# Optimization experiments

Hardware: AMD Instinct MI355X
Metric: run time of the kernel (lower is better)

The kernel has to match this reference:

```python
import jax, jax.numpy as jnp
import numpy as np

T, D, E, DE = 50000, 128, 1600000, 3
EPS = 1e-5


def setup_inputs() -> dict:
    key = jax.random.key(0)
    ks = jax.random.split(key, 8)
    H = jax.random.normal(ks[0], (T, D), dtype=jnp.float32)
    edge_index = jax.random.randint(ks[1], (2, E), 0, T, dtype=jnp.int64)
    edge_attr = jax.random.normal(ks[2], (E, DE), dtype=jnp.float32)
    # phi: Linear(D+DE -> D), GELU, Linear(D -> D)
    s1 = 1.0 / np.sqrt(D + DE)
    s2 = 1.0 / np.sqrt(D)
    W1 = jax.random.uniform(ks[3], (D + DE, D), minval=-s1, maxval=s1, dtype=jnp.float32)
    b1 = jax.random.uniform(ks[4], (D,), minval=-s1, maxval=s1, dtype=jnp.float32)
    W2 = jax.random.uniform(ks[5], (D, D), minval=-s2, maxval=s2, dtype=jnp.float32)
    b2 = jax.random.uniform(ks[6], (D,), minval=-s2, maxval=s2, dtype=jnp.float32)
    gamma = jnp.ones((D,), dtype=jnp.float32)
    beta = jnp.zeros((D,), dtype=jnp.float32)
    return {"H": H, "edge_index": edge_index, "edge_attr": edge_attr,
            "W1": W1, "b1": b1, "W2": W2, "b2": b2, "gamma": gamma, "beta": beta}


def reference(H, edge_index, edge_attr, W1, b1, W2, b2, gamma, beta):
    src, dst = edge_index[0], edge_index[1]
    Hj = H[src]                                   # [E, D] gather
    feat = jnp.concatenate([Hj, edge_attr], axis=-1)  # [E, D+DE]
    h = jax.nn.gelu(feat @ W1 + b1, approximate=False)
    m = h @ W2 + b2                               # [E, D] messages
    agg = jax.ops.segment_sum(m, dst, num_segments=H.shape[0])  # scatter-add
    x = H + agg
    mu = jnp.mean(x, axis=-1, keepdims=True)
    var = jnp.mean((x - mu) ** 2, axis=-1, keepdims=True)
    return (x - mu) * jax.lax.rsqrt(var + EPS) * gamma + beta
```

## Files before the change

### kernel.cpp

```cpp
#include <hip/hip_runtime.h>
#include <hip/hip_bf16.h>

typedef unsigned short u16;
typedef unsigned int u32;
typedef __attribute__((ext_vector_type(8))) __bf16 bf16x8;
typedef __attribute__((ext_vector_type(4))) float f32x4;

#define NT 50000
#define NEDGE 1600000
#define GRID2 2048
#define NPAIR 4096
#define NBIN 50176

__device__ __forceinline__ u16 f2bf(float f) {
  unsigned x = __float_as_uint(f);
  x += 0x7fffu + ((x >> 16) & 1u);
  return (u16)(x >> 16);
}

__device__ __forceinline__ int swz(int row, int col) {
  return (row << 7) + (col ^ ((row & 7) << 3));
}

__device__ __forceinline__ float gelu(float v) {
  float u = v * v;
  float arg = v * __builtin_fmaf(-0.1029434f, u, -2.3022082f);
  float e = __builtin_amdgcn_exp2f(arg);
  return v * __builtin_amdgcn_rcpf(1.0f + e);
}

__device__ __forceinline__ void atomAddF32(float* p, float v) {
#if defined(__has_builtin)
#if __has_builtin(__builtin_amdgcn_global_atomic_fadd_f32)
  __builtin_amdgcn_global_atomic_fadd_f32((__attribute__((address_space(1))) float*)p, v);
  return;
#endif
#endif
  atomicAdd(p, v);
}


__global__ void prep_all(const float* __restrict__ H, u16* __restrict__ Hb,
                         const float* __restrict__ W1, const float* __restrict__ W2,
                         u16* __restrict__ wsw, const float* __restrict__ b1,
                         u16* __restrict__ wx, u32* __restrict__ cnt) {
  int bid = blockIdx.x, tid = threadIdx.x;
  if (bid < 3125) {
    int t = bid * 256 + tid;
    const float4* s = (const float4*)H + (long)t * 2;
    float4 a = s[0], c = s[1];
    int4 pk;
    pk.x = f2bf(a.x) | ((int)f2bf(a.y) << 16);
    pk.y = f2bf(a.z) | ((int)f2bf(a.w) << 16);
    pk.z = f2bf(c.x) | ((int)f2bf(c.y) << 16);
    pk.w = f2bf(c.z) | ((int)f2bf(c.w) << 16);
    ((int4*)Hb)[t] = pk;
  } else if (bid < 3253) {
    int t = (bid - 3125) * 256 + tid;
    int m = t >> 14;
    int p = t & 16383;
    int row = p >> 7;
    int colq = p & 127;
    int k = colq ^ ((row & 7) << 3);
    const float* W = m ? W2 : W1;
    wsw[t] = f2bf(W[k * 128 + row]);
  } else if (bid < 3257) {
    int t = (bid - 3253) * 256 + tid;
    int row = t >> 3, j = t & 7;
    float v = 0.f;
    if (j < 3) v = W1[(128 + j) * 128 + row];
    else if (j == 3) v = b1[row];
    wx[t] = f2bf(v);
  } else if (bid < 3453) {
    int t = (bid - 3257) * 256 + tid;
    if (t < NBIN) cnt[t] = 0;
  } else {
    if (tid < 16) ((int4*)(Hb + (long)NT * 128))[tid] = make_int4(0, 0, 0, 0);
  }
}

__global__ void copy_h(const float4* __restrict__ H, float4* __restrict__ out) {
  int t = blockIdx.x * 256 + threadIdx.x;
  out[t] = H[t];
}


__global__ void hist_g(const int* __restrict__ ei, u32* __restrict__ cnt) {
  int e = blockIdx.x * 256 + threadIdx.x;
  atomicAdd(&cnt[ei[NEDGE + e]], 1u);
}

__global__ void scan_blk(u32* __restrict__ cnt, u32* __restrict__ btot) {
  __shared__ u32 ls[1024];
  int tid = threadIdx.x;
  int bin = blockIdx.x * 1024 + tid;
  u32 c = cnt[bin];
  ls[tid] = c;
  __syncthreads();
  for (int o = 1; o < 1024; o <<= 1) {
    u32 t = (tid >= o) ? ls[tid - o] : 0u;
    __syncthreads();
    ls[tid] += t;
    __syncthreads();
  }
  cnt[bin] = ls[tid] - c;
  if (tid == 1023) btot[blockIdx.x] = ls[1023];
}

__global__ void scan_btot(u32* __restrict__ btot) {
  if (threadIdx.x == 0) {
    u32 run = 0;
    for (int i = 0; i < 49; ++i) { u32 t = btot[i]; btot[i] = run; run += t; }
  }
}

__global__ void fin_base(const u32* __restrict__ cnt, const u32* __restrict__ btot,
                         u32* __restrict__ base, u32* __restrict__ pos) {
  int bin = blockIdx.x * 256 + threadIdx.x;
  if (bin < NT) {
    u32 v = cnt[bin] + btot[bin >> 10];
    base[bin] = v;
    pos[bin] = v;
  }
  if (bin == NT) base[NT] = NEDGE;
}

__global__ void scatter_g(const int* __restrict__ ei, const float* __restrict__ ea,
                          u32* __restrict__ pos, uint2* __restrict__ rec) {
  int e = blockIdx.x * 256 + threadIdx.x;
  int d = ei[NEDGE + e];
  int s = ei[e];
  float e0 = ea[e * 3 + 0], e1 = ea[e * 3 + 1], e2 = ea[e * 3 + 2];
  u32 p = atomicAdd(&pos[d], 1u);
  rec[p] = make_uint2((u32)s | ((u32)f2bf(e0) << 16),
                      (u32)f2bf(e1) | ((u32)f2bf(e2) << 16));
}


__launch_bounds__(256)
__global__ void msg_agg(const u16* __restrict__ Hb,
                        const u16* __restrict__ wsw,
                        const u16* __restrict__ wx,
                        const u32* __restrict__ base,
                        const uint2* __restrict__ rec,
                        u16* __restrict__ hsb) {
  __shared__ __align__(16) u16 lw1x[128 * 8];

  const int tid = threadIdx.x;
  if (tid < 128) ((int4*)lw1x)[tid] = ((const int4*)wx)[tid];
  __syncthreads();

  const int wv = tid >> 6, lane = tid & 63;
  const int l15 = lane & 15, l4 = lane >> 4;

  const int gid = blockIdx.x * 4 + wv;
  const int pair = gid >> 1;
  const int nh = gid & 1;

  bf16x8 af[4][4];
#pragma unroll
  for (int nt = 0; nt < 4; ++nt)
#pragma unroll
    for (int ks = 0; ks < 4; ++ks)
      af[nt][ks] = *(const bf16x8*)&wsw[swz((nh * 4 + nt) * 16 + l15, ks * 32 + l4 * 8)];

  const int d0 = (int)(((long)pair * NT) / NPAIR);
  const int d1i = (int)(((long)(pair + 1) * NT) / NPAIR);
  const int nd = d1i - d0;

  for (int b = 0; b < nd; ++b) {
    const int start = (int)base[d0 + b];
    const int cnt = (int)base[d0 + b + 1] - start;

    float racc[4][4];
#pragma unroll
    for (int nt = 0; nt < 4; ++nt)
#pragma unroll
      for (int r = 0; r < 4; ++r) racc[nt][r] = 0.f;

    const int ntile = (cnt + 15) >> 4;
    uint2 r2c = make_uint2(0, 0);
    if (ntile > 0) {
      int i0 = (l15 < cnt) ? l15 : cnt - 1;
      r2c = rec[start + i0];
    }

    for (int t = 0; t < ntile; ++t) {
      int inx = (t + 1) * 16 + l15;
      if (inx >= cnt) inx = cnt - 1;
      uint2 r2n = rec[start + inx];

      const bool valid = (t * 16 + l15) < cnt;
      int src = valid ? (int)(r2c.x & 0xFFFFu) : NT;
      u32 x0 = 0u, x1 = 0u;
      if (l4 == 0 && valid) {
        x0 = (r2c.x >> 16) | (r2c.y << 16);
        x1 = (r2c.y >> 16) | 0x3F800000u;
      }
      int4 xbi = make_int4((int)x0, (int)x1, 0, 0);
      bf16x8 bfrx = *(bf16x8*)&xbi;

      bf16x8 bfc[4];
      {
        const u16* hr = Hb + (long)src * 128;
#pragma unroll
        for (int ks = 0; ks < 4; ++ks)
          bfc[ks] = *(const bf16x8*)(hr + ks * 32 + l4 * 8);
      }

#pragma unroll
      for (int nt = 0; nt < 4; ++nt) {
        bf16x8 afrx = *(const bf16x8*)&lw1x[((nh * 4 + nt) * 16 + l15) * 8];
        f32x4 acc = (f32x4){0.f, 0.f, 0.f, 0.f};
#pragma unroll
        for (int ks = 0; ks < 4; ++ks)
          acc = __builtin_amdgcn_mfma_f32_16x16x32_bf16(bfc[ks], af[nt][ks], acc, 0, 0, 0);
        acc = __builtin_amdgcn_mfma_f32_16x16x32_bf16(bfrx, afrx, acc, 0, 0, 0);
#pragma unroll
        for (int r = 0; r < 4; ++r)
          racc[nt][r] += gelu(acc[r]);
      }
      r2c = r2n;
    }

    float sv[4];
#pragma unroll
    for (int nt = 0; nt < 4; ++nt) {
      float s = racc[nt][0] + racc[nt][1] + racc[nt][2] + racc[nt][3];
      s += __shfl_xor(s, 16);
      s += __shfl_xor(s, 32);
      sv[nt] = s;
    }
    float sa = (l4 == 0) ? sv[0] : (l4 == 1) ? sv[1] : (l4 == 2) ? sv[2] : sv[3];
    u16* hrow = hsb + (long)(d0 + b) * 128;
    hrow[nh * 64 + l4 * 16 + l15] = f2bf(sa);
  }
}


__launch_bounds__(256)
__global__ void gemm_ln(const u16* __restrict__ hsb,
                        const float* __restrict__ H,
                        const float* __restrict__ b2,
                        const u16* __restrict__ wsw,
                        const u32* __restrict__ base,
                        const float* __restrict__ gamma,
                        const float* __restrict__ beta,
                        float* __restrict__ out) {
  __shared__ __align__(16) u16 lw2[16384];
  const int tid = threadIdx.x;
  {
    const int4* g = (const int4*)wsw + 2048;
    int4* d2 = (int4*)lw2;
#pragma unroll
    for (int i = 0; i < 8; ++i) { int c = tid + i * 256; d2[c] = g[c]; }
  }
  __syncthreads();

  const int wv = tid >> 6, lane = tid & 63;
  const int l15 = lane & 15, l4 = lane >> 4;
  const int r0 = (blockIdx.x * 4 + wv) * 16;

  bf16x8 ha[4];
#pragma unroll
  for (int ks = 0; ks < 4; ++ks)
    ha[ks] = *(const bf16x8*)(hsb + (long)(r0 + l15) * 128 + ks * 32 + l4 * 8);

  float cntr[4];
#pragma unroll
  for (int r = 0; r < 4; ++r) {
    int row = r0 + l4 * 4 + r;
    if (row > NT - 1) row = NT - 1;
    cntr[r] = (float)(base[row + 1] - base[row]);
  }

  float xv[8][4];
#pragma unroll
  for (int nt = 0; nt < 8; ++nt) {
    bf16x8 bfr2[4];
#pragma unroll
    for (int ks = 0; ks < 4; ++ks)
      bfr2[ks] = *(const bf16x8*)&lw2[swz(nt * 16 + l15, ks * 32 + l4 * 8)];
    float b2v = b2[nt * 16 + l15];
    f32x4 acc = (f32x4){0.f, 0.f, 0.f, 0.f};
#pragma unroll
    for (int ks = 0; ks < 4; ++ks)
      acc = __builtin_amdgcn_mfma_f32_16x16x32_bf16(ha[ks], bfr2[ks], acc, 0, 0, 0);
#pragma unroll
    for (int r = 0; r < 4; ++r) {
      int row = r0 + l4 * 4 + r;
      long o = (long)((row < NT) ? row : NT - 1) * 128 + nt * 16 + l15;
      xv[nt][r] = H[o] + acc[r] + cntr[r] * b2v;
    }
  }

  float mu[4], rs[4];
#pragma unroll
  for (int r = 0; r < 4; ++r) {
    float s = 0.f;
#pragma unroll
    for (int nt = 0; nt < 8; ++nt) s += xv[nt][r];
    s += __shfl_xor(s, 1); s += __shfl_xor(s, 2);
    s += __shfl_xor(s, 4); s += __shfl_xor(s, 8);
    mu[r] = s * (1.0f / 128.0f);
    float q = 0.f;
#pragma unroll
    for (int nt = 0; nt < 8; ++nt) {
      float d = xv[nt][r] - mu[r];
      q += d * d;
    }
    q += __shfl_xor(q, 1); q += __shfl_xor(q, 2);
    q += __shfl_xor(q, 4); q += __shfl_xor(q, 8);
    rs[r] = rsqrtf(q * (1.0f / 128.0f) + 1e-5f);
  }

#pragma unroll
  for (int nt = 0; nt < 8; ++nt) {
    int col = nt * 16 + l15;
    float g = gamma[col], bb = beta[col];
#pragma unroll
    for (int r = 0; r < 4; ++r) {
      int row = r0 + l4 * 4 + r;
      if (row < NT)
        out[(long)row * 128 + col] = (xv[nt][r] - mu[r]) * rs[r] * g + bb;
    }
  }
}


template <int BF16H>
__launch_bounds__(256, 1)
__global__ void msg_atomic(const float* __restrict__ H,
                           const u16* __restrict__ Hb,
                           const int* __restrict__ ei,
                           const float* __restrict__ ea,
                           const float* __restrict__ W1,
                           const float* __restrict__ b1,
                           const float* __restrict__ b2,
                           const u16* __restrict__ wsw,
                           float* __restrict__ out) {
  __shared__ __align__(16) u16 lw1[16384];
  __shared__ __align__(16) u16 lw2[16384];
  __shared__ __align__(16) u16 lh[4 * 2048];
  __shared__ __align__(16) float lep[5][128];

  const int tid = threadIdx.x;
  {
    const int4* g = (const int4*)wsw;
    int4* d1 = (int4*)lw1;
    int4* d2 = (int4*)lw2;
#pragma unroll
    for (int i = 0; i < 8; ++i) {
      int c = tid + i * 256;
      d1[c] = g[c];
      d2[c] = g[2048 + c];
    }
  }
  if (tid < 128) {
    lep[0][tid] = b1[tid];
    lep[1][tid] = W1[128 * 128 + tid];
    lep[2][tid] = W1[129 * 128 + tid];
    lep[3][tid] = W1[130 * 128 + tid];
    lep[4][tid] = b2[tid];
  }
  __syncthreads();

  const int wv = tid >> 6, lane = tid & 63;
  const int l15 = lane & 15, l4 = lane >> 4;
  u16* lhw = lh + wv * 2048;
  const int gwid = blockIdx.x * 4 + wv;

  for (int g = gwid; g < NEDGE / 16; g += 4096) {
    const int eb = g * 16;
    int src = ei[eb + l15];
    float ea0 = ea[(eb + l15) * 3 + 0], ea1 = ea[(eb + l15) * 3 + 1], ea2 = ea[(eb + l15) * 3 + 2];

    bf16x8 bfr[4];
    if (BF16H) {
      const u16* hr = Hb + (long)src * 128;
#pragma unroll
      for (int ks = 0; ks < 4; ++ks)
        bfr[ks] = *(const bf16x8*)(hr + ks * 32 + l4 * 8);
    } else {
      const float* hr = H + (long)src * 128;
#pragma unroll
      for (int ks = 0; ks < 4; ++ks) {
        float4 a = *(const float4*)(hr + ks * 32 + l4 * 8);
        float4 c = *(const float4*)(hr + ks * 32 + l4 * 8 + 4);
        int4 pk;
        pk.x = f2bf(a.x) | ((int)f2bf(a.y) << 16);
        pk.y = f2bf(a.z) | ((int)f2bf(a.w) << 16);
        pk.z = f2bf(c.x) | ((int)f2bf(c.y) << 16);
        pk.w = f2bf(c.z) | ((int)f2bf(c.w) << 16);
        bfr[ks] = *(bf16x8*)&pk;
      }
    }

#pragma unroll
    for (int nt = 0; nt < 8; ++nt) {
      bf16x8 afr[4];
#pragma unroll
      for (int ks = 0; ks < 4; ++ks)
        afr[ks] = *(const bf16x8*)&lw1[swz(nt * 16 + l15, ks * 32 + l4 * 8)];
      f32x4 acc = (f32x4){0.f, 0.f, 0.f, 0.f};
#pragma unroll
      for (int ks = 0; ks < 4; ++ks)
        acc = __builtin_amdgcn_mfma_f32_16x16x32_bf16(afr[ks], bfr[ks], acc, 0, 0, 0);
      f32x4 b1v = *(const f32x4*)&lep[0][nt * 16 + l4 * 4];
      f32x4 w0v = *(const f32x4*)&lep[1][nt * 16 + l4 * 4];
      f32x4 w1v = *(const f32x4*)&lep[2][nt * 16 + l4 * 4];
      f32x4 w2v = *(const f32x4*)&lep[3][nt * 16 + l4 * 4];
      float hv[4];
#pragma unroll
      for (int r = 0; r < 4; ++r) {
        float v = acc[r] + b1v[r] + ea0 * w0v[r] + ea1 * w1v[r] + ea2 * w2v[r];
        hv[r] = gelu(v);
      }
      int2 hp;
      hp.x = f2bf(hv[0]) | ((int)f2bf(hv[1]) << 16);
      hp.y = f2bf(hv[2]) | ((int)f2bf(hv[3]) << 16);
      *(int2*)&lhw[swz(l15, nt * 16 + l4 * 4)] = hp;
    }

    asm volatile("" ::: "memory");

    bf16x8 ha[4];
#pragma unroll
    for (int ks = 0; ks < 4; ++ks)
      ha[ks] = *(const bf16x8*)&lhw[swz(l15, ks * 32 + l4 * 8)];
    int drow[4];
#pragma unroll
    for (int r = 0; r < 4; ++r) drow[r] = ei[NEDGE + eb + l4 * 4 + r];

#pragma unroll
    for (int nt = 0; nt < 8; ++nt) {
      bf16x8 bfr2[4];
#pragma unroll
      for (int ks = 0; ks < 4; ++ks)
        bfr2[ks] = *(const bf16x8*)&lw2[swz(nt * 16 + l15, ks * 32 + l4 * 8)];
      float b2v = lep[4][nt * 16 + l15];
      f32x4 acc = (f32x4){0.f, 0.f, 0.f, 0.f};
#pragma unroll
      for (int ks = 0; ks < 4; ++ks)
        acc = __builtin_amdgcn_mfma_f32_16x16x32_bf16(ha[ks], bfr2[ks], acc, 0, 0, 0);
#pragma unroll
      for (int r = 0; r < 4; ++r)
        atomAddF32(out + (long)drow[r] * 128 + nt * 16 + l15, acc[r] + b2v);
    }
  }
}

__global__ void ln_rows(float* __restrict__ out, const float* __restrict__ gamma,
                        const float* __restrict__ beta) {
  int wave = threadIdx.x >> 6, lane = threadIdx.x & 63;
  int row = blockIdx.x * 4 + wave;
  float2 v = *(const float2*)(out + (long)row * 128 + lane * 2);
  float s = v.x + v.y;
#pragma unroll
  for (int off = 32; off; off >>= 1) s += __shfl_xor(s, off);
  float mu = s * (1.0f / 128.0f);
  float dx = v.x - mu, dy = v.y - mu;
  float q = dx * dx + dy * dy;
#pragma unroll
  for (int off = 32; off; off >>= 1) q += __shfl_xor(q, off);
  float rs = rsqrtf(q * (1.0f / 128.0f) + 1e-5f);
  float2 g = *(const float2*)(gamma + lane * 2);
  float2 b = *(const float2*)(beta + lane * 2);
  float2 o;
  o.x = dx * rs * g.x + b.x;
  o.y = dy * rs * g.y + b.y;
  *(float2*)(out + (long)row * 128 + lane * 2) = o;
}

extern "C" void kernel_launch(void* const* d_in, const int* in_sizes, int n_in,
                              void* d_out, int out_size, void* d_ws, size_t ws_size,
                              hipStream_t stream) {
  const float* H   = (const float*)d_in[0];
  const int* ei    = (const int*)d_in[1];
  const float* ea  = (const float*)d_in[2];
  const float* W1  = (const float*)d_in[3];
  const float* b1  = (const float*)d_in[4];
  const float* W2  = (const float*)d_in[5];
  const float* b2  = (const float*)d_in[6];
  const float* gam = (const float*)d_in[7];
  const float* bet = (const float*)d_in[8];
  float* out = (float*)d_out;

  char* ws = (char*)d_ws;
  u16* wsw   = (u16*)ws;
  u16* wx    = (u16*)(ws + 65536);
  u16* Hb    = (u16*)(ws + 67584);
  u32* cnt   = (u32*)(ws + 12867840);
  u32* base  = (u32*)(ws + 13068544);
  u32* pos   = (u32*)(ws + 13268560);
  u32* btot  = (u32*)(ws + 13468560);
  uint2* rec = (uint2*)(ws + 13468832);
  u16* hsb   = (u16*)(ws + 26268832);
  const size_t NEED_FULL = 39081120;
  const size_t NEED_HB = 12867840;

  if (ws_size >= NEED_FULL) {
    prep_all<<<3454, 256, 0, stream>>>(H, Hb, W1, W2, wsw, b1, wx, cnt);
    hist_g<<<6250, 256, 0, stream>>>(ei, cnt);
    scan_blk<<<49, 1024, 0, stream>>>(cnt, btot);
    scan_btot<<<1, 64, 0, stream>>>(btot);
    fin_base<<<196, 256, 0, stream>>>(cnt, btot, base, pos);
    scatter_g<<<6250, 256, 0, stream>>>(ei, ea, pos, rec);
    msg_agg<<<GRID2, 256, 0, stream>>>(Hb, wsw, wx, base, rec, hsb);
    gemm_ln<<<782, 256, 0, stream>>>(hsb, H, b2, wsw, base, gam, bet, out);
  } else if (ws_size >= NEED_HB) {
    prep_all<<<3454, 256, 0, stream>>>(H, Hb, W1, W2, wsw, b1, wx, cnt);
    copy_h<<<6250, 256, 0, stream>>>((const float4*)H, (float4*)out);
    msg_atomic<1><<<1024, 256, 0, stream>>>(H, Hb, ei, ea, W1, b1, b2, wsw, out);
    ln_rows<<<12500, 256, 0, stream>>>(out, gam, bet);
  } else {
    copy_h<<<6250, 256, 0, stream>>>((const float4*)H, (float4*)out);
    msg_atomic<0><<<1024, 256, 0, stream>>>(H, Hb, ei, ea, W1, b1, b2, wsw, out);
    ln_rows<<<12500, 256, 0, stream>>>(out, gam, bet);
  }
}
```

Before: 372.8 us.

## Edge-balanced msg_agg with packed multi-destination tiles and fused btot scan

Rewrites msg_agg so each wave takes an equal slice of the CSR edge range, found by binary search over base, instead of a fixed range of destinations. Tiles of 16 edges can now span several destinations, and per-row masks split the GELU outputs among them. This removes the padding waste from partial tiles and the load imbalance between waves. Each wave now covers all 128 output columns and reads W1 fragments from global or cache per tile rather than holding them in registers. It also prefetches the next tile's H rows and folds the single-thread btot scan into fin_base, saving one launch. The costs are more register pressure, repeated weight loads, and extra masking FMAs per tile.

```diff
diff --git a/kernel.cpp b/kernel.cpp
--- a/kernel.cpp
+++ b/kernel.cpp
@@ -9,7 +9,7 @@
 #define NT 50000
 #define NEDGE 1600000
 #define GRID2 2048
-#define NPAIR 4096
+#define TOTW 8192
 #define NBIN 50176
 
 __device__ __forceinline__ u16 f2bf(float f) {
@@ -107,18 +107,18 @@
   if (tid == 1023) btot[blockIdx.x] = ls[1023];
 }
 
-__global__ void scan_btot(u32* __restrict__ btot) {
-  if (threadIdx.x == 0) {
-    u32 run = 0;
-    for (int i = 0; i < 49; ++i) { u32 t = btot[i]; btot[i] = run; run += t; }
-  }
-}
-
 __global__ void fin_base(const u32* __restrict__ cnt, const u32* __restrict__ btot,
                          u32* __restrict__ base, u32* __restrict__ pos) {
-  int bin = blockIdx.x * 256 + threadIdx.x;
+  __shared__ u32 bpre[49];
+  int tid = threadIdx.x;
+  if (tid == 0) {
+    u32 run = 0;
+    for (int i = 0; i < 49; ++i) { u32 t = btot[i]; bpre[i] = run; run += t; }
+  }
+  __syncthreads();
+  int bin = blockIdx.x * 256 + tid;
   if (bin < NT) {
-    u32 v = cnt[bin] + btot[bin >> 10];
+    u32 v = cnt[bin] + bpre[bin >> 10];
     base[bin] = v;
     pos[bin] = v;
   }
@@ -137,7 +137,7 @@
 }
 
 
-__launch_bounds__(256)
+__launch_bounds__(256, 1)
 __global__ void msg_agg(const u16* __restrict__ Hb,
                         const u16* __restrict__ wsw,
                         const u16* __restrict__ wx,
@@ -152,88 +152,127 @@
 
   const int wv = tid >> 6, lane = tid & 63;
   const int l15 = lane & 15, l4 = lane >> 4;
-
   const int gid = blockIdx.x * 4 + wv;
-  const int pair = gid >> 1;
-  const int nh = gid & 1;
-
-  bf16x8 af[4][4];
-#pragma unroll
-  for (int nt = 0; nt < 4; ++nt)
+
+  const long t0 = ((long)gid * NEDGE) / TOTW;
+  const long t1 = ((long)(gid + 1) * NEDGE) / TOTW;
+  int lo = 0, hi = NT;
+  while (lo < hi) { int mid = (lo + hi) >> 1; if ((long)base[mid] < t0) lo = mid + 1; else hi = mid; }
+  const int d0 = lo;
+  hi = NT;
+  while (lo < hi) { int mid = (lo + hi) >> 1; if ((long)base[mid] < t1) lo = mid + 1; else hi = mid; }
+  const int d1i = lo;
+  if (d0 >= d1i) return;
+
+  const int pstart = (int)base[d0];
+  const int pend = (int)base[d1i];
+  int bcur = d0;
+  int tlo = pstart;
+  int cend = (int)base[d0 + 1];
+
+  float racc[8][4];
+#pragma unroll
+  for (int nt = 0; nt < 8; ++nt)
+#pragma unroll
+    for (int r = 0; r < 4; ++r) racc[nt][r] = 0.f;
+
+  int pp = pstart + l15;
+  bool vc0 = pp < pend;
+  if (!vc0) pp = pend - 1;
+  uint2 r2c = rec[pp];
+  bf16x8 bfc[4];
+  {
+    int src0 = vc0 ? (int)(r2c.x & 0xFFFFu) : NT;
+    const u16* hr = Hb + (long)src0 * 128;
 #pragma unroll
     for (int ks = 0; ks < 4; ++ks)
-      af[nt][ks] = *(const bf16x8*)&wsw[swz((nh * 4 + nt) * 16 + l15, ks * 32 + l4 * 8)];
-
-  const int d0 = (int)(((long)pair * NT) / NPAIR);
-  const int d1i = (int)(((long)(pair + 1) * NT) / NPAIR);
-  const int nd = d1i - d0;
-
-  for (int b = 0; b < nd; ++b) {
-    const int start = (int)base[d0 + b];
-    const int cnt = (int)base[d0 + b + 1] - start;
-
-    float racc[4][4];
-#pragma unroll
-    for (int nt = 0; nt < 4; ++nt)
-#pragma unroll
-      for (int r = 0; r < 4; ++r) racc[nt][r] = 0.f;
-
-    const int ntile = (cnt + 15) >> 4;
-    uint2 r2c = make_uint2(0, 0);
-    if (ntile > 0) {
-      int i0 = (l15 < cnt) ? l15 : cnt - 1;
-      r2c = rec[start + i0];
-    }
-
-    for (int t = 0; t < ntile; ++t) {
-      int inx = (t + 1) * 16 + l15;
-      if (inx >= cnt) inx = cnt - 1;
-      uint2 r2n = rec[start + inx];
-
-      const bool valid = (t * 16 + l15) < cnt;
-      int src = valid ? (int)(r2c.x & 0xFFFFu) : NT;
-      u32 x0 = 0u, x1 = 0u;
-      if (l4 == 0 && valid) {
-        x0 = (r2c.x >> 16) | (r2c.y << 16);
-        x1 = (r2c.y >> 16) | 0x3F800000u;
+      bfc[ks] = *(const bf16x8*)(hr + ks * 32 + l4 * 8);
+  }
+
+  for (int p0 = pstart; p0 < pend; p0 += 16) {
+    int pn = p0 + 16 + l15;
+    bool vn = pn < pend;
+    if (!vn) pn = pend - 1;
+    uint2 r2n = rec[pn];
+    bf16x8 bfn[4];
+    {
+      int srcn = vn ? (int)(r2n.x & 0xFFFFu) : NT;
+      const u16* hr = Hb + (long)srcn * 128;
+#pragma unroll
+      for (int ks = 0; ks < 4; ++ks)
+        bfn[ks] = *(const bf16x8*)(hr + ks * 32 + l4 * 8);
+    }
+
+    bool vc = (p0 + l15) < pend;
+    u32 x0 = 0u, x1 = 0u;
+    if (l4 == 0 && vc) {
+      x0 = (r2c.x >> 16) | (r2c.y << 16);
+      x1 = (r2c.y >> 16) | 0x3F800000u;
+    }
+    int4 xbi = make_int4((int)x0, (int)x1, 0, 0);
+    bf16x8 bfrx = *(bf16x8*)&xbi;
+
+    float gv[8][4];
+#pragma unroll
+    for (int nt = 0; nt < 8; ++nt) {
+      bf16x8 afrx = *(const bf16x8*)&lw1x[(nt * 16 + l15) * 8];
+      f32x4 acc = (f32x4){0.f, 0.f, 0.f, 0.f};
+#pragma unroll
+      for (int ks = 0; ks < 4; ++ks) {
+        bf16x8 afr = *(const bf16x8*)&wsw[swz(nt * 16 + l15, ks * 32 + l4 * 8)];
+        acc = __builtin_amdgcn_mfma_f32_16x16x32_bf16(bfc[ks], afr, acc, 0, 0, 0);
       }
-      int4 xbi = make_int4((int)x0, (int)x1, 0, 0);
-      bf16x8 bfrx = *(bf16x8*)&xbi;
-
-      bf16x8 bfc[4];
-      {
-        const u16* hr = Hb + (long)src * 128;
-#pragma unroll
-        for (int ks = 0; ks < 4; ++ks)
-          bfc[ks] = *(const bf16x8*)(hr + ks * 32 + l4 * 8);
+      acc = __builtin_amdgcn_mfma_f32_16x16x32_bf16(bfrx, afrx, acc, 0, 0, 0);
+#pragma unroll
+      for (int r = 0; r < 4; ++r)
+        gv[nt][r] = gelu(acc[r]);
+    }
+
+    int thi = p0 + 16;
+    if (thi > pend) thi = pend;
+    while (true) {
+      float m[4];
+#pragma unroll
+      for (int r = 0; r < 4; ++r) {
+        int pos = p0 + l4 * 4 + r;
+        m[r] = (pos >= tlo && pos < cend) ? 1.0f : 0.0f;
       }
-
-#pragma unroll
-      for (int nt = 0; nt < 4; ++nt) {
-        bf16x8 afrx = *(const bf16x8*)&lw1x[((nh * 4 + nt) * 16 + l15) * 8];
-        f32x4 acc = (f32x4){0.f, 0.f, 0.f, 0.f};
-#pragma unroll
-        for (int ks = 0; ks < 4; ++ks)
-          acc = __builtin_amdgcn_mfma_f32_16x16x32_bf16(bfc[ks], af[nt][ks], acc, 0, 0, 0);
-        acc = __builtin_amdgcn_mfma_f32_16x16x32_bf16(bfrx, afrx, acc, 0, 0, 0);
+#pragma unroll
+      for (int nt = 0; nt < 8; ++nt)
 #pragma unroll
         for (int r = 0; r < 4; ++r)
-          racc[nt][r] += gelu(acc[r]);
+          racc[nt][r] = __builtin_fmaf(gv[nt][r], m[r], racc[nt][r]);
+
+      if (cend > thi) break;
+
+      float sv[8];
+#pragma unroll
+      for (int nt = 0; nt < 8; ++nt) {
+        float s = racc[nt][0] + racc[nt][1] + racc[nt][2] + racc[nt][3];
+        s += __shfl_xor(s, 16);
+        s += __shfl_xor(s, 32);
+        sv[nt] = s;
       }
-      r2c = r2n;
-    }
-
-    float sv[4];
-#pragma unroll
-    for (int nt = 0; nt < 4; ++nt) {
-      float s = racc[nt][0] + racc[nt][1] + racc[nt][2] + racc[nt][3];
-      s += __shfl_xor(s, 16);
-      s += __shfl_xor(s, 32);
-      sv[nt] = s;
-    }
-    float sa = (l4 == 0) ? sv[0] : (l4 == 1) ? sv[1] : (l4 == 2) ? sv[2] : sv[3];
-    u16* hrow = hsb + (long)(d0 + b) * 128;
-    hrow[nh * 64 + l4 * 16 + l15] = f2bf(sa);
+      float sa = (l4 == 0) ? sv[0] : (l4 == 1) ? sv[1] : (l4 == 2) ? sv[2] : sv[3];
+      float sb = (l4 == 0) ? sv[4] : (l4 == 1) ? sv[5] : (l4 == 2) ? sv[6] : sv[7];
+      u16* hrow = hsb + (long)bcur * 128;
+      hrow[l4 * 16 + l15] = f2bf(sa);
+      hrow[64 + l4 * 16 + l15] = f2bf(sb);
+#pragma unroll
+      for (int nt = 0; nt < 8; ++nt)
+#pragma unroll
+        for (int r = 0; r < 4; ++r) racc[nt][r] = 0.f;
+
+      tlo = cend;
+      ++bcur;
+      if (bcur >= d1i) break;
+      cend = (int)base[bcur + 1];
+      if (tlo >= thi) break;
+    }
+
+    r2c = r2n;
+#pragma unroll
+    for (int ks = 0; ks < 4; ++ks) bfc[ks] = bfn[ks];
   }
 }
 
@@ -503,7 +542,6 @@
     prep_all<<<3454, 256, 0, stream>>>(H, Hb, W1, W2, wsw, b1, wx, cnt);
     hist_g<<<6250, 256, 0, stream>>>(ei, cnt);
     scan_blk<<<49, 1024, 0, stream>>>(cnt, btot);
-    scan_btot<<<1, 64, 0, stream>>>(btot);
     fin_base<<<196, 256, 0, stream>>>(cnt, btot, base, pos);
     scatter_g<<<6250, 256, 0, stream>>>(ei, ea, pos, rec);
     msg_agg<<<GRID2, 256, 0, stream>>>(Hb, wsw, wx, base, rec, hsb);
```

Measured after the change: 427.4 us. 1.15x slower.
